# Optimization experiments

Measured on AMD Instinct MI355X. Metric: run time of the kernel, lower is better.

Reference implementation:

```python
import jax, jax.numpy as jnp
import numpy as np

N, E, F, H = 50000, 1_600_000, 6, 64


def setup_inputs() -> dict:
    key = jax.random.key(0)
    ks = jax.random.split(key, 12)
    inp = {
        "vertex_features": jax.random.normal(ks[0], (N, F), dtype=jnp.float32),
        "edges": jax.random.randint(ks[1], (2, E), 0, N, dtype=jnp.int64 if jax.config.jax_enable_x64 else jnp.int32),
        "weights": jax.random.uniform(ks[2], (E,), dtype=jnp.float32),
        # GCNConv layer params (glorot-ish scale) + biases (PyG default bias=True)
        "W1": jax.random.normal(ks[3], (F, H), dtype=jnp.float32) / np.sqrt(F),
        "b1": jnp.zeros((H,), jnp.float32),
        "W2": jax.random.normal(ks[4], (H, H), dtype=jnp.float32) / np.sqrt(H),
        "b2": jnp.zeros((H,), jnp.float32),
        "W3": jax.random.normal(ks[5], (H, H), dtype=jnp.float32) / np.sqrt(H),
        "b3": jnp.zeros((H,), jnp.float32),
        "Wl": jax.random.normal(ks[6], (H, 1), dtype=jnp.float32) / np.sqrt(H),
        "bl": jnp.zeros((1,), jnp.float32),
    }
    return inp


def _gcn_norm(edges, weights, n):
    # PyG gcn_norm: add self loops (weight 1), symmetric D^-1/2 A D^-1/2;
    # degree computed at target nodes (edge_index[1], flow source_to_target).
    row, col = edges[0], edges[1]
    loop = jnp.arange(n, dtype=row.dtype)
    row_f = jnp.concatenate([row, loop])
    col_f = jnp.concatenate([col, loop])
    w_f = jnp.concatenate([weights, jnp.ones((n,), weights.dtype)])
    deg = jax.ops.segment_sum(w_f, col_f, num_segments=n)
    dis = jnp.where(deg > 0, jax.lax.rsqrt(jnp.maximum(deg, 1e-30)), 0.0)
    norm = dis[row_f] * w_f * dis[col_f]
    return row_f, col_f, norm


def _gcn_conv(x, W, b, row, col, norm, n):
    xw = x @ W                                   # [n, H_out]
    agg = jax.ops.segment_sum(norm[:, None] * xw[row], col, num_segments=n)
    return agg + b


def reference(vertex_features, edges, weights, W1, b1, W2, b2, W3, b3, Wl, bl):
    n = vertex_features.shape[0]
    row, col, norm = _gcn_norm(edges, weights, n)  # norm identical for all layers
    h = jax.nn.sigmoid(_gcn_conv(vertex_features, W1, b1, row, col, norm, n))
    h = jax.nn.sigmoid(_gcn_conv(h, W2, b2, row, col, norm, n))
    h = jax.nn.sigmoid(_gcn_conv(h, W3, b3, row, col, norm, n))
    logits = h @ Wl + bl                           # [n, 1]
    return jax.nn.softmax(logits, axis=0)          # softmax over node dim
```

## Files before the change

### kernel.cpp

```cpp
#include <hip/hip_runtime.h>
#include <math.h>


#define BLK 256
#define SKB 256
#define CHUNK 4096

typedef __attribute__((ext_vector_type(8))) short bf16x8;
typedef __attribute__((ext_vector_type(4))) float f32x4;

__device__ inline unsigned short f2bf(float f) {
  unsigned u = __float_as_uint(f);
  return (unsigned short)((u + 0x7FFF + ((u >> 16) & 1)) >> 16);
}
__device__ inline float bflo(unsigned u) { return __uint_as_float(u << 16); }
__device__ inline float bfhi(unsigned u) { return __uint_as_float(u & 0xFFFF0000u); }


__global__ __launch_bounds__(256) void k_binscatter(
    const int* __restrict__ row, const int* __restrict__ col,
    const float* __restrict__ w, int E,
    int* __restrict__ bfill, int2* __restrict__ bucket, int CAP) {
  __shared__ int2 stage[CHUNK];
  __shared__ int lhist[SKB], lbase[SKB], gbase[SKB], lfill[SKB];
  int t = threadIdx.x;
  int e0 = blockIdx.x * CHUNK;
  int n = E - e0; if (n > CHUNK) n = CHUNK;
  lhist[t] = 0; lfill[t] = 0;
  __syncthreads();
  for (int i = t; i < n; i += BLK) atomicAdd(&lhist[((unsigned)col[e0 + i]) >> 8], 1);
  __syncthreads();
  lbase[t] = lhist[t];
  __syncthreads();
  for (int off = 1; off < SKB; off <<= 1) {
    int v = (t >= off) ? lbase[t - off] : 0;
    __syncthreads();
    lbase[t] += v;
    __syncthreads();
  }
  int excl = lbase[t] - lhist[t];
  int cb = lhist[t];
  gbase[t] = cb ? atomicAdd(&bfill[t << 4], cb) : 0;
  __syncthreads();
  lbase[t] = excl;
  __syncthreads();
  for (int i = t; i < n; i += BLK) {
    int c = col[e0 + i];
    int b = ((unsigned)c) >> 8;
    int r = atomicAdd(&lfill[b], 1);
    stage[lbase[b] + r] = make_int2(row[e0 + i] | (c << 16), __float_as_int(w[e0 + i]));
  }
  __syncthreads();
  for (int i = t; i < n; i += BLK) {
    int2 p = stage[i];
    int b = ((unsigned)p.x) >> 24;
    bucket[(size_t)b * CAP + gbase[b] + (i - lbase[b])] = p;
  }
}


__global__ __launch_bounds__(256) void k_build(
    const int2* __restrict__ bucket, const int* __restrict__ bfill,
    const float* __restrict__ x,
    unsigned* __restrict__ csr, int* __restrict__ cnt, int* __restrict__ start,
    float* __restrict__ dis, unsigned short* __restrict__ x8b, int CAP, int N) {
  __shared__ int   hist[SKB];
  __shared__ float wsum[SKB];
  __shared__ int   lstart[SKB + 1];
  __shared__ int   lfill[SKB];
  int b = blockIdx.x, t = threadIdx.x;
  int n0 = b << 8;
  int M = N - n0; if (M > 256) M = 256;
  if (M <= 0) return;
  hist[t] = 0; wsum[t] = 0.0f; lfill[t] = 0;
  __syncthreads();
  const int2* bb = bucket + (size_t)b * CAP;
  int ec = bfill[b << 4];
  for (int i = t; i < ec; i += BLK) {
    int2 p = bb[i];
    int lc = (((unsigned)p.x) >> 16) & 255;
    atomicAdd(&hist[lc], 1);
    atomicAdd(&wsum[lc], __int_as_float(p.y));
  }
  __syncthreads();
  if (t == 0) {
    int run = 0;
    for (int i = 0; i < M; ++i) { lstart[i] = run; run += hist[i]; }
    lstart[M] = run;
  }
  __syncthreads();
  if (t < M) {
    int n = n0 + t;
    cnt[n] = hist[t];
    start[n] = b * CAP + lstart[t];
    float d = 1.0f / sqrtf(wsum[t] + 1.0f);
    dis[n] = d;
    const float* xr = x + (size_t)n * 6;
    uint4 pk;
    pk.x = (unsigned)f2bf(d * xr[0]) | ((unsigned)f2bf(d * xr[1]) << 16);
    pk.y = (unsigned)f2bf(d * xr[2]) | ((unsigned)f2bf(d * xr[3]) << 16);
    pk.z = (unsigned)f2bf(d * xr[4]) | ((unsigned)f2bf(d * xr[5]) << 16);
    pk.w = 0u;
    *(uint4*)(x8b + (size_t)n * 8) = pk;
  }
  __syncthreads();
  for (int i = t; i < ec; i += BLK) {
    int2 p = bb[i];
    int lc = (((unsigned)p.x) >> 16) & 255;
    int pos = lstart[lc] + atomicAdd(&lfill[lc], 1);
    csr[(size_t)b * CAP + pos] =
        ((unsigned)p.x & 0xFFFFu) | ((unsigned)f2bf(__int_as_float(p.y)) << 16);
  }
}


__global__ void k_wprep(const float* __restrict__ W2, const float* __restrict__ W3,
                        unsigned short* __restrict__ W2b, unsigned short* __restrict__ W3b) {
  int i = blockIdx.x * blockDim.x + threadIdx.x;
  if (i < 4096) { W2b[i] = f2bf(W2[i]); W3b[i] = f2bf(W3[i]); }
}


__global__ void k_layer1(const unsigned short* __restrict__ x8b,
                         const int* __restrict__ start, const int* __restrict__ cnt,
                         const unsigned* __restrict__ csr, const float* __restrict__ dis,
                         const float* __restrict__ W1, const float* __restrict__ b1,
                         unsigned short* __restrict__ hb, int N) {
  int t = blockIdx.x * blockDim.x + threadIdx.x;
  int n = t >> 3, sub = t & 7;
  if (n >= N) return;
  float a0 = 0.f, a1 = 0.f, a2 = 0.f, a3 = 0.f, a4 = 0.f, a5 = 0.f;
  if (sub == 0) {
    uint4 sv = *(const uint4*)(x8b + (size_t)n * 8);
    a0 = bflo(sv.x); a1 = bfhi(sv.x); a2 = bflo(sv.y);
    a3 = bfhi(sv.y); a4 = bflo(sv.z); a5 = bfhi(sv.z);
  }
  int s = start[n], e = s + cnt[n];
  int i = s + sub;
  for (; i + 8 < e; i += 16) {
    unsigned p0 = csr[i], p1 = csr[i + 8];
    uint4 h0 = *(const uint4*)(x8b + (size_t)(p0 & 0xFFFFu) * 8);
    uint4 h1 = *(const uint4*)(x8b + (size_t)(p1 & 0xFFFFu) * 8);
    float v0 = bfhi(p0), v1 = bfhi(p1);
    a0 += v0 * bflo(h0.x) + v1 * bflo(h1.x);
    a1 += v0 * bfhi(h0.x) + v1 * bfhi(h1.x);
    a2 += v0 * bflo(h0.y) + v1 * bflo(h1.y);
    a3 += v0 * bfhi(h0.y) + v1 * bfhi(h1.y);
    a4 += v0 * bflo(h0.z) + v1 * bflo(h1.z);
    a5 += v0 * bfhi(h0.z) + v1 * bfhi(h1.z);
  }
  for (; i < e; i += 8) {
    unsigned pe = csr[i];
    float v = bfhi(pe);
    uint4 hv = *(const uint4*)(x8b + (size_t)(pe & 0xFFFFu) * 8);
    a0 += v * bflo(hv.x); a1 += v * bfhi(hv.x);
    a2 += v * bflo(hv.y); a3 += v * bfhi(hv.y);
    a4 += v * bflo(hv.z); a5 += v * bfhi(hv.z);
  }
#pragma unroll
  for (int m = 1; m < 8; m <<= 1) {
    a0 += __shfl_xor(a0, m, 64); a1 += __shfl_xor(a1, m, 64);
    a2 += __shfl_xor(a2, m, 64); a3 += __shfl_xor(a3, m, 64);
    a4 += __shfl_xor(a4, m, 64); a5 += __shfl_xor(a5, m, 64);
  }
  float d = dis[n];
  a0 *= d; a1 *= d; a2 *= d; a3 *= d; a4 *= d; a5 *= d;
  unsigned short* o = hb + (size_t)n * 64;
#pragma unroll
  for (int jj = 0; jj < 2; ++jj) {
    int j4 = sub * 2 + jj;
    float4 acc = *(const float4*)(b1 + j4 * 4);
    const float* Wc = W1 + j4 * 4;
    acc.x += a0*Wc[0] + a1*Wc[64] + a2*Wc[128] + a3*Wc[192] + a4*Wc[256] + a5*Wc[320];
    acc.y += a0*Wc[1] + a1*Wc[65] + a2*Wc[129] + a3*Wc[193] + a4*Wc[257] + a5*Wc[321];
    acc.z += a0*Wc[2] + a1*Wc[66] + a2*Wc[130] + a3*Wc[194] + a4*Wc[258] + a5*Wc[322];
    acc.w += a0*Wc[3] + a1*Wc[67] + a2*Wc[131] + a3*Wc[195] + a4*Wc[259] + a5*Wc[323];
    uint2 pk;
    pk.x = (unsigned)f2bf(d / (1.0f + expf(-acc.x))) |
           ((unsigned)f2bf(d / (1.0f + expf(-acc.y))) << 16);
    pk.y = (unsigned)f2bf(d / (1.0f + expf(-acc.z))) |
           ((unsigned)f2bf(d / (1.0f + expf(-acc.w))) << 16);
    *(uint2*)(o + j4 * 4) = pk;
  }
}


__global__ void k_agg64(const unsigned short* __restrict__ hb,
                        const int* __restrict__ start, const int* __restrict__ cnt,
                        const unsigned* __restrict__ csr, const float* __restrict__ dis,
                        unsigned short* __restrict__ aggb, int N) {
  int t = blockIdx.x * blockDim.x + threadIdx.x;
  int n = t >> 4, sub = t & 15;
  if (n >= N) return;
  uint2 sv = *(const uint2*)(hb + (size_t)n * 64 + sub * 4);
  float a0 = bflo(sv.x), a1 = bfhi(sv.x), a2 = bflo(sv.y), a3 = bfhi(sv.y);
  int s = start[n], e = s + cnt[n];
  int i = s;
  for (; i + 8 <= e; i += 8) {
    unsigned p0 = csr[i],     p1 = csr[i + 1], p2 = csr[i + 2], p3 = csr[i + 3];
    unsigned p4 = csr[i + 4], p5 = csr[i + 5], p6 = csr[i + 6], p7 = csr[i + 7];
    uint2 h0 = *(const uint2*)(hb + (size_t)(p0 & 0xFFFFu) * 64 + sub * 4);
    uint2 h1 = *(const uint2*)(hb + (size_t)(p1 & 0xFFFFu) * 64 + sub * 4);
    uint2 h2 = *(const uint2*)(hb + (size_t)(p2 & 0xFFFFu) * 64 + sub * 4);
    uint2 h3 = *(const uint2*)(hb + (size_t)(p3 & 0xFFFFu) * 64 + sub * 4);
    uint2 h4 = *(const uint2*)(hb + (size_t)(p4 & 0xFFFFu) * 64 + sub * 4);
    uint2 h5 = *(const uint2*)(hb + (size_t)(p5 & 0xFFFFu) * 64 + sub * 4);
    uint2 h6 = *(const uint2*)(hb + (size_t)(p6 & 0xFFFFu) * 64 + sub * 4);
    uint2 h7 = *(const uint2*)(hb + (size_t)(p7 & 0xFFFFu) * 64 + sub * 4);
    float v0 = bfhi(p0), v1 = bfhi(p1), v2 = bfhi(p2), v3 = bfhi(p3);
    float v4 = bfhi(p4), v5 = bfhi(p5), v6 = bfhi(p6), v7 = bfhi(p7);
    a0 += v0*bflo(h0.x) + v1*bflo(h1.x) + v2*bflo(h2.x) + v3*bflo(h3.x)
        + v4*bflo(h4.x) + v5*bflo(h5.x) + v6*bflo(h6.x) + v7*bflo(h7.x);
    a1 += v0*bfhi(h0.x) + v1*bfhi(h1.x) + v2*bfhi(h2.x) + v3*bfhi(h3.x)
        + v4*bfhi(h4.x) + v5*bfhi(h5.x) + v6*bfhi(h6.x) + v7*bfhi(h7.x);
    a2 += v0*bflo(h0.y) + v1*bflo(h1.y) + v2*bflo(h2.y) + v3*bflo(h3.y)
        + v4*bflo(h4.y) + v5*bflo(h5.y) + v6*bflo(h6.y) + v7*bflo(h7.y);
    a3 += v0*bfhi(h0.y) + v1*bfhi(h1.y) + v2*bfhi(h2.y) + v3*bfhi(h3.y)
        + v4*bfhi(h4.y) + v5*bfhi(h5.y) + v6*bfhi(h6.y) + v7*bfhi(h7.y);
  }
  for (; i < e; ++i) {
    unsigned pe = csr[i];
    float v = bfhi(pe);
    uint2 hv = *(const uint2*)(hb + (size_t)(pe & 0xFFFFu) * 64 + sub * 4);
    a0 += v * bflo(hv.x); a1 += v * bfhi(hv.x);
    a2 += v * bflo(hv.y); a3 += v * bfhi(hv.y);
  }
  float d = dis[n];
  uint2 pk;
  pk.x = (unsigned)f2bf(d * a0) | ((unsigned)f2bf(d * a1) << 16);
  pk.y = (unsigned)f2bf(d * a2) | ((unsigned)f2bf(d * a3) << 16);
  *(uint2*)(aggb + (size_t)n * 64 + sub * 4) = pk;
}


__global__ __launch_bounds__(256) void k_dense64_mfma(
    const unsigned short* __restrict__ aggb, const unsigned short* __restrict__ Wb,
    const float* __restrict__ b, const float* __restrict__ dis,
    unsigned short* __restrict__ hb, int NS) {
  int wid = threadIdx.x >> 6, lane = threadIdx.x & 63;
  int quad = lane >> 4, r16 = lane & 15;
  bf16x8 Bf[2][4];
#pragma unroll
  for (int kt = 0; kt < 2; ++kt)
#pragma unroll
    for (int jt = 0; jt < 4; ++jt)
#pragma unroll
      for (int j = 0; j < 8; ++j)
        Bf[kt][jt][j] = (short)Wb[(kt * 32 + quad * 8 + j) * 64 + jt * 16 + r16];
  float bias[4];
#pragma unroll
  for (int jt = 0; jt < 4; ++jt) bias[jt] = b[jt * 16 + r16];
  int stride = gridDim.x * 4;
  for (int s = blockIdx.x * 4 + wid; s < NS; s += stride) {
    int n0 = s * 16;
    bf16x8 Af0 = *(const bf16x8*)(aggb + (size_t)(n0 + r16) * 64 + quad * 8);
    bf16x8 Af1 = *(const bf16x8*)(aggb + (size_t)(n0 + r16) * 64 + 32 + quad * 8);
    f32x4 C[4];
#pragma unroll
    for (int jt = 0; jt < 4; ++jt) {
      f32x4 z = {0.f, 0.f, 0.f, 0.f};
      z = __builtin_amdgcn_mfma_f32_16x16x32_bf16(Af0, Bf[0][jt], z, 0, 0, 0);
      z = __builtin_amdgcn_mfma_f32_16x16x32_bf16(Af1, Bf[1][jt], z, 0, 0, 0);
      C[jt] = z;
    }
    float dv[4];
#pragma unroll
    for (int reg = 0; reg < 4; ++reg) dv[reg] = dis[n0 + quad * 4 + reg];
#pragma unroll
    for (int jt = 0; jt < 4; ++jt)
#pragma unroll
      for (int reg = 0; reg < 4; ++reg) {
        float h = dv[reg] / (1.0f + expf(-(C[jt][reg] + bias[jt])));
        hb[(size_t)(n0 + quad * 4 + reg) * 64 + jt * 16 + r16] = f2bf(h);
      }
  }
}


__global__ __launch_bounds__(256) void k_head_mfma(
    const unsigned short* __restrict__ aggb, const unsigned short* __restrict__ Wb,
    const float* __restrict__ b, const float* __restrict__ Wl,
    const float* __restrict__ bl, float* __restrict__ expv,
    float* __restrict__ red_part, int NS) {
  int wid = threadIdx.x >> 6, lane = threadIdx.x & 63;
  int quad = lane >> 4, r16 = lane & 15;
  bf16x8 Bf[2][4];
#pragma unroll
  for (int kt = 0; kt < 2; ++kt)
#pragma unroll
    for (int jt = 0; jt < 4; ++jt)
#pragma unroll
      for (int j = 0; j < 8; ++j)
        Bf[kt][jt][j] = (short)Wb[(kt * 32 + quad * 8 + j) * 64 + jt * 16 + r16];
  float bias[4], wlv[4];
#pragma unroll
  for (int jt = 0; jt < 4; ++jt) {
    bias[jt] = b[jt * 16 + r16];
    wlv[jt]  = Wl[jt * 16 + r16];
  }
  float bl0 = bl[0];
  float lsum = 0.0f;
  int stride = gridDim.x * 4;
  for (int s = blockIdx.x * 4 + wid; s < NS; s += stride) {
    int n0 = s * 16;
    bf16x8 Af0 = *(const bf16x8*)(aggb + (size_t)(n0 + r16) * 64 + quad * 8);
    bf16x8 Af1 = *(const bf16x8*)(aggb + (size_t)(n0 + r16) * 64 + 32 + quad * 8);
    f32x4 C[4];
#pragma unroll
    for (int jt = 0; jt < 4; ++jt) {
      f32x4 z = {0.f, 0.f, 0.f, 0.f};
      z = __builtin_amdgcn_mfma_f32_16x16x32_bf16(Af0, Bf[0][jt], z, 0, 0, 0);
      z = __builtin_amdgcn_mfma_f32_16x16x32_bf16(Af1, Bf[1][jt], z, 0, 0, 0);
      C[jt] = z;
    }
    float p0 = 0, p1 = 0, p2 = 0, p3 = 0;
#pragma unroll
    for (int jt = 0; jt < 4; ++jt) {
      p0 += wlv[jt] / (1.0f + expf(-(C[jt][0] + bias[jt])));
      p1 += wlv[jt] / (1.0f + expf(-(C[jt][1] + bias[jt])));
      p2 += wlv[jt] / (1.0f + expf(-(C[jt][2] + bias[jt])));
      p3 += wlv[jt] / (1.0f + expf(-(C[jt][3] + bias[jt])));
    }
#pragma unroll
    for (int m = 1; m < 16; m <<= 1) {
      p0 += __shfl_xor(p0, m, 64);
      p1 += __shfl_xor(p1, m, 64);
      p2 += __shfl_xor(p2, m, 64);
      p3 += __shfl_xor(p3, m, 64);
    }
    float ls = 0.0f;
    if (r16 == 0) {
      float e0 = expf(p0 + bl0), e1 = expf(p1 + bl0);
      float e2 = expf(p2 + bl0), e3 = expf(p3 + bl0);
      int r = n0 + quad * 4;
      expv[r] = e0; expv[r + 1] = e1; expv[r + 2] = e2; expv[r + 3] = e3;
      ls = e0 + e1 + e2 + e3;
    }
    ls += __shfl_xor(ls, 16, 64);
    ls += __shfl_xor(ls, 32, 64);
    lsum += ls;
  }
  if (lane == 0) atomicAdd(&red_part[(blockIdx.x & 63) << 4], lsum);
}

__global__ void k_out(const float* __restrict__ expv, int N,
                      const float* __restrict__ red_part, float* __restrict__ out) {
  int i = blockIdx.x * blockDim.x + threadIdx.x;
  int lane = threadIdx.x & 63;
  float s = red_part[lane << 4];
#pragma unroll
  for (int o = 32; o > 0; o >>= 1) s += __shfl_down(s, o, 64);
  s = __shfl(s, 0, 64);
  if (i < N) out[i] = expv[i] / s;
}


extern "C" void kernel_launch(void* const* d_in, const int* in_sizes, int n_in,
                              void* d_out, int out_size, void* d_ws, size_t ws_size,
                              hipStream_t stream) {
  const float* x   = (const float*)d_in[0];
  const int*   edg = (const int*)d_in[1];
  const float* w   = (const float*)d_in[2];
  const float* W1  = (const float*)d_in[3];
  const float* b1  = (const float*)d_in[4];
  const float* W2  = (const float*)d_in[5];
  const float* b2  = (const float*)d_in[6];
  const float* W3  = (const float*)d_in[7];
  const float* b3  = (const float*)d_in[8];
  const float* Wl  = (const float*)d_in[9];
  const float* bl  = (const float*)d_in[10];
  float* out = (float*)d_out;

  const int N = in_sizes[0] / 6;
  const int E = in_sizes[2];
  const int* row = edg;
  const int* col = edg + E;
  const int NB = (N + 255) >> 8;
  const int NS = (N + 15) / 16;

  size_t off = 0;
  char* base = (char*)d_ws;
  auto alloc = [&](size_t bytes) -> void* {
    void* p = base + off;
    off += (bytes + 255) & ~(size_t)255;
    return p;
  };
  int*   bfill    = (int*)alloc((size_t)SKB * 16 * 4);
  float* red_part = (float*)alloc((size_t)64 * 16 * 4);
  size_t zero_bytes = off;
  int*   cnt    = (int*)alloc((size_t)N * 4);
  int*   start  = (int*)alloc((size_t)N * 4);
  float* dis    = (float*)alloc((size_t)N * 4);
  float* expv   = (float*)alloc((size_t)N * 4);
  unsigned short* x8b = (unsigned short*)alloc((size_t)N * 8 * 2);
  unsigned short* hb  = (unsigned short*)alloc((size_t)N * 64 * 2);
  unsigned short* W2b = (unsigned short*)alloc(4096 * 2);
  unsigned short* W3b = (unsigned short*)alloc(4096 * 2);
  size_t remain = (ws_size > off) ? (ws_size - off) : 0;
  long long capn = ((long long)remain) / ((long long)NB * 12);
  int CAP = (int)capn;
  if (CAP > 9216) CAP = 9216;
  if (CAP < 8704) CAP = 8704;
  unsigned* csr = (unsigned*)alloc((size_t)NB * CAP * 4);
  size_t aggsz = (size_t)N * 64 * 2;
  size_t bksz  = (size_t)NB * CAP * 8;
  void* shared_blk = alloc(aggsz > bksz ? aggsz : bksz);
  int2*           bucket = (int2*)shared_blk;
  unsigned short* aggb   = (unsigned short*)shared_blk;

  const int gE   = (E + CHUNK - 1) / CHUNK;
  const int gN   = (N + BLK - 1) / BLK;
  const int gN8  = (N * 8 + BLK - 1) / BLK;
  const int gN16 = (N * 16 + BLK - 1) / BLK;
  const int gM   = 200;

  hipMemsetAsync(d_ws, 0, zero_bytes, stream);

  k_wprep     <<<16, BLK, 0, stream>>>(W2, W3, W2b, W3b);
  k_binscatter<<<gE, BLK, 0, stream>>>(row, col, w, E, bfill, bucket, CAP);
  k_build     <<<NB, BLK, 0, stream>>>(bucket, bfill, x, csr, cnt, start, dis, x8b, CAP, N);

  k_layer1<<<gN8, BLK, 0, stream>>>(x8b, start, cnt, csr, dis, W1, b1, hb, N);

  k_agg64       <<<gN16, BLK, 0, stream>>>(hb, start, cnt, csr, dis, aggb, N);
  k_dense64_mfma<<<gM,   BLK, 0, stream>>>(aggb, W2b, b2, dis, hb, NS);

  k_agg64    <<<gN16, BLK, 0, stream>>>(hb, start, cnt, csr, dis, aggb, N);
  k_head_mfma<<<gM,   BLK, 0, stream>>>(aggb, W3b, b3, Wl, bl, expv, red_part, NS);

  k_out<<<gN, BLK, 0, stream>>>(expv, N, red_part, out);
}
```

Before: 234.7 us.

## Fuse neighbor aggregation with MFMA dense transform per 16-node tile

Merges the separate aggregation and MFMA dense kernels for layers 2 and 3 into single kernels. Each block aggregates 16 nodes into padded shared memory, then runs the 64x64 bf16 MFMA and sigmoid, and for the last layer also the head, exp and partial sum. This removes the global round trip of the aggregated buffer and two launches. Layer 2 now writes to a separate buffer that reuses the bucket space, because other blocks still read the input features. The weight-conversion kernel is folded into extra blocks of the bin-scatter launch. The trade-off is that each block now reloads W from global memory and the head does more atomics, one per 16 nodes.

```diff
diff --git a/kernel.cpp b/kernel.cpp
--- a/kernel.cpp
+++ b/kernel.cpp
@@ -5,6 +5,7 @@
 #define BLK 256
 #define SKB 256
 #define CHUNK 4096
+#define LROW 72
 
 typedef __attribute__((ext_vector_type(8))) short bf16x8;
 typedef __attribute__((ext_vector_type(4))) float f32x4;
@@ -20,7 +21,14 @@
 __global__ __launch_bounds__(256) void k_binscatter(
     const int* __restrict__ row, const int* __restrict__ col,
     const float* __restrict__ w, int E,
-    int* __restrict__ bfill, int2* __restrict__ bucket, int CAP) {
+    int* __restrict__ bfill, int2* __restrict__ bucket, int CAP, int nEB,
+    const float* __restrict__ W2, const float* __restrict__ W3,
+    unsigned short* __restrict__ W2b, unsigned short* __restrict__ W3b) {
+  if (blockIdx.x >= nEB) {
+    int i = (blockIdx.x - nEB) * BLK + threadIdx.x;
+    if (i < 4096) { W2b[i] = f2bf(W2[i]); W3b[i] = f2bf(W3[i]); }
+    return;
+  }
   __shared__ int2 stage[CHUNK];
   __shared__ int lhist[SKB], lbase[SKB], gbase[SKB], lfill[SKB];
   int t = threadIdx.x;
@@ -114,13 +122,6 @@
 }
 
 
-__global__ void k_wprep(const float* __restrict__ W2, const float* __restrict__ W3,
-                        unsigned short* __restrict__ W2b, unsigned short* __restrict__ W3b) {
-  int i = blockIdx.x * blockDim.x + threadIdx.x;
-  if (i < 4096) { W2b[i] = f2bf(W2[i]); W3b[i] = f2bf(W3[i]); }
-}
-
-
 __global__ void k_layer1(const unsigned short* __restrict__ x8b,
                          const int* __restrict__ start, const int* __restrict__ cnt,
                          const unsigned* __restrict__ csr, const float* __restrict__ dis,
@@ -185,162 +186,143 @@
 }
 
 
-__global__ void k_agg64(const unsigned short* __restrict__ hb,
-                        const int* __restrict__ start, const int* __restrict__ cnt,
-                        const unsigned* __restrict__ csr, const float* __restrict__ dis,
-                        unsigned short* __restrict__ aggb, int N) {
-  int t = blockIdx.x * blockDim.x + threadIdx.x;
-  int n = t >> 4, sub = t & 15;
-  if (n >= N) return;
-  uint2 sv = *(const uint2*)(hb + (size_t)n * 64 + sub * 4);
-  float a0 = bflo(sv.x), a1 = bfhi(sv.x), a2 = bflo(sv.y), a3 = bfhi(sv.y);
-  int s = start[n], e = s + cnt[n];
-  int i = s;
-  for (; i + 8 <= e; i += 8) {
-    unsigned p0 = csr[i],     p1 = csr[i + 1], p2 = csr[i + 2], p3 = csr[i + 3];
-    unsigned p4 = csr[i + 4], p5 = csr[i + 5], p6 = csr[i + 6], p7 = csr[i + 7];
-    uint2 h0 = *(const uint2*)(hb + (size_t)(p0 & 0xFFFFu) * 64 + sub * 4);
-    uint2 h1 = *(const uint2*)(hb + (size_t)(p1 & 0xFFFFu) * 64 + sub * 4);
-    uint2 h2 = *(const uint2*)(hb + (size_t)(p2 & 0xFFFFu) * 64 + sub * 4);
-    uint2 h3 = *(const uint2*)(hb + (size_t)(p3 & 0xFFFFu) * 64 + sub * 4);
-    uint2 h4 = *(const uint2*)(hb + (size_t)(p4 & 0xFFFFu) * 64 + sub * 4);
-    uint2 h5 = *(const uint2*)(hb + (size_t)(p5 & 0xFFFFu) * 64 + sub * 4);
-    uint2 h6 = *(const uint2*)(hb + (size_t)(p6 & 0xFFFFu) * 64 + sub * 4);
-    uint2 h7 = *(const uint2*)(hb + (size_t)(p7 & 0xFFFFu) * 64 + sub * 4);
-    float v0 = bfhi(p0), v1 = bfhi(p1), v2 = bfhi(p2), v3 = bfhi(p3);
-    float v4 = bfhi(p4), v5 = bfhi(p5), v6 = bfhi(p6), v7 = bfhi(p7);
-    a0 += v0*bflo(h0.x) + v1*bflo(h1.x) + v2*bflo(h2.x) + v3*bflo(h3.x)
-        + v4*bflo(h4.x) + v5*bflo(h5.x) + v6*bflo(h6.x) + v7*bflo(h7.x);
-    a1 += v0*bfhi(h0.x) + v1*bfhi(h1.x) + v2*bfhi(h2.x) + v3*bfhi(h3.x)
-        + v4*bfhi(h4.x) + v5*bfhi(h5.x) + v6*bfhi(h6.x) + v7*bfhi(h7.x);
-    a2 += v0*bflo(h0.y) + v1*bflo(h1.y) + v2*bflo(h2.y) + v3*bflo(h3.y)
-        + v4*bflo(h4.y) + v5*bflo(h5.y) + v6*bflo(h6.y) + v7*bflo(h7.y);
-    a3 += v0*bfhi(h0.y) + v1*bfhi(h1.y) + v2*bfhi(h2.y) + v3*bfhi(h3.y)
-        + v4*bfhi(h4.y) + v5*bfhi(h5.y) + v6*bfhi(h6.y) + v7*bfhi(h7.y);
-  }
-  for (; i < e; ++i) {
-    unsigned pe = csr[i];
-    float v = bfhi(pe);
-    uint2 hv = *(const uint2*)(hb + (size_t)(pe & 0xFFFFu) * 64 + sub * 4);
-    a0 += v * bflo(hv.x); a1 += v * bfhi(hv.x);
-    a2 += v * bflo(hv.y); a3 += v * bfhi(hv.y);
-  }
-  float d = dis[n];
-  uint2 pk;
-  pk.x = (unsigned)f2bf(d * a0) | ((unsigned)f2bf(d * a1) << 16);
-  pk.y = (unsigned)f2bf(d * a2) | ((unsigned)f2bf(d * a3) << 16);
-  *(uint2*)(aggb + (size_t)n * 64 + sub * 4) = pk;
-}
-
-
-__global__ __launch_bounds__(256) void k_dense64_mfma(
-    const unsigned short* __restrict__ aggb, const unsigned short* __restrict__ Wb,
-    const float* __restrict__ b, const float* __restrict__ dis,
-    unsigned short* __restrict__ hb, int NS) {
-  int wid = threadIdx.x >> 6, lane = threadIdx.x & 63;
-  int quad = lane >> 4, r16 = lane & 15;
-  bf16x8 Bf[2][4];
-#pragma unroll
-  for (int kt = 0; kt < 2; ++kt)
-#pragma unroll
-    for (int jt = 0; jt < 4; ++jt)
-#pragma unroll
-      for (int j = 0; j < 8; ++j)
-        Bf[kt][jt][j] = (short)Wb[(kt * 32 + quad * 8 + j) * 64 + jt * 16 + r16];
-  float bias[4];
-#pragma unroll
-  for (int jt = 0; jt < 4; ++jt) bias[jt] = b[jt * 16 + r16];
-  int stride = gridDim.x * 4;
-  for (int s = blockIdx.x * 4 + wid; s < NS; s += stride) {
-    int n0 = s * 16;
-    bf16x8 Af0 = *(const bf16x8*)(aggb + (size_t)(n0 + r16) * 64 + quad * 8);
-    bf16x8 Af1 = *(const bf16x8*)(aggb + (size_t)(n0 + r16) * 64 + 32 + quad * 8);
-    f32x4 C[4];
-#pragma unroll
-    for (int jt = 0; jt < 4; ++jt) {
-      f32x4 z = {0.f, 0.f, 0.f, 0.f};
-      z = __builtin_amdgcn_mfma_f32_16x16x32_bf16(Af0, Bf[0][jt], z, 0, 0, 0);
-      z = __builtin_amdgcn_mfma_f32_16x16x32_bf16(Af1, Bf[1][jt], z, 0, 0, 0);
-      C[jt] = z;
+__device__ inline void agg16(const unsigned short* __restrict__ hb,
+                             const int* __restrict__ start,
+                             const int* __restrict__ cnt,
+                             const unsigned* __restrict__ csr,
+                             const float* __restrict__ dis,
+                             unsigned short* lag, int n0, int N) {
+  int t = threadIdx.x;
+  int r = t >> 4, sub = t & 15;
+  int n = n0 + r;
+  uint2 pk = make_uint2(0u, 0u);
+  if (n < N) {
+    uint2 sv = *(const uint2*)(hb + (size_t)n * 64 + sub * 4);
+    float a0 = bflo(sv.x), a1 = bfhi(sv.x), a2 = bflo(sv.y), a3 = bfhi(sv.y);
+    int s = start[n], e = s + cnt[n];
+    int i = s;
+    for (; i + 8 <= e; i += 8) {
+      unsigned p0 = csr[i],     p1 = csr[i + 1], p2 = csr[i + 2], p3 = csr[i + 3];
+      unsigned p4 = csr[i + 4], p5 = csr[i + 5], p6 = csr[i + 6], p7 = csr[i + 7];
+      uint2 h0 = *(const uint2*)(hb + (size_t)(p0 & 0xFFFFu) * 64 + sub * 4);
+      uint2 h1 = *(const uint2*)(hb + (size_t)(p1 & 0xFFFFu) * 64 + sub * 4);
+      uint2 h2 = *(const uint2*)(hb + (size_t)(p2 & 0xFFFFu) * 64 + sub * 4);
+      uint2 h3 = *(const uint2*)(hb + (size_t)(p3 & 0xFFFFu) * 64 + sub * 4);
+      uint2 h4 = *(const uint2*)(hb + (size_t)(p4 & 0xFFFFu) * 64 + sub * 4);
+      uint2 h5 = *(const uint2*)(hb + (size_t)(p5 & 0xFFFFu) * 64 + sub * 4);
+      uint2 h6 = *(const uint2*)(hb + (size_t)(p6 & 0xFFFFu) * 64 + sub * 4);
+      uint2 h7 = *(const uint2*)(hb + (size_t)(p7 & 0xFFFFu) * 64 + sub * 4);
+      float v0 = bfhi(p0), v1 = bfhi(p1), v2 = bfhi(p2), v3 = bfhi(p3);
+      float v4 = bfhi(p4), v5 = bfhi(p5), v6 = bfhi(p6), v7 = bfhi(p7);
+      a0 += v0*bflo(h0.x) + v1*bflo(h1.x) + v2*bflo(h2.x) + v3*bflo(h3.x)
+          + v4*bflo(h4.x) + v5*bflo(h5.x) + v6*bflo(h6.x) + v7*bflo(h7.x);
+      a1 += v0*bfhi(h0.x) + v1*bfhi(h1.x) + v2*bfhi(h2.x) + v3*bfhi(h3.x)
+          + v4*bfhi(h4.x) + v5*bfhi(h5.x) + v6*bfhi(h6.x) + v7*bfhi(h7.x);
+      a2 += v0*bflo(h0.y) + v1*bflo(h1.y) + v2*bflo(h2.y) + v3*bflo(h3.y)
+          + v4*bflo(h4.y) + v5*bflo(h5.y) + v6*bflo(h6.y) + v7*bflo(h7.y);
+      a3 += v0*bfhi(h0.y) + v1*bfhi(h1.y) + v2*bfhi(h2.y) + v3*bfhi(h3.y)
+          + v4*bfhi(h4.y) + v5*bfhi(h5.y) + v6*bfhi(h6.y) + v7*bfhi(h7.y);
     }
-    float dv[4];
-#pragma unroll
-    for (int reg = 0; reg < 4; ++reg) dv[reg] = dis[n0 + quad * 4 + reg];
-#pragma unroll
-    for (int jt = 0; jt < 4; ++jt)
-#pragma unroll
-      for (int reg = 0; reg < 4; ++reg) {
-        float h = dv[reg] / (1.0f + expf(-(C[jt][reg] + bias[jt])));
-        hb[(size_t)(n0 + quad * 4 + reg) * 64 + jt * 16 + r16] = f2bf(h);
-      }
-  }
-}
-
-
-__global__ __launch_bounds__(256) void k_head_mfma(
-    const unsigned short* __restrict__ aggb, const unsigned short* __restrict__ Wb,
-    const float* __restrict__ b, const float* __restrict__ Wl,
-    const float* __restrict__ bl, float* __restrict__ expv,
-    float* __restrict__ red_part, int NS) {
-  int wid = threadIdx.x >> 6, lane = threadIdx.x & 63;
-  int quad = lane >> 4, r16 = lane & 15;
-  bf16x8 Bf[2][4];
-#pragma unroll
-  for (int kt = 0; kt < 2; ++kt)
-#pragma unroll
-    for (int jt = 0; jt < 4; ++jt)
-#pragma unroll
-      for (int j = 0; j < 8; ++j)
-        Bf[kt][jt][j] = (short)Wb[(kt * 32 + quad * 8 + j) * 64 + jt * 16 + r16];
-  float bias[4], wlv[4];
-#pragma unroll
-  for (int jt = 0; jt < 4; ++jt) {
-    bias[jt] = b[jt * 16 + r16];
-    wlv[jt]  = Wl[jt * 16 + r16];
-  }
-  float bl0 = bl[0];
-  float lsum = 0.0f;
-  int stride = gridDim.x * 4;
-  for (int s = blockIdx.x * 4 + wid; s < NS; s += stride) {
-    int n0 = s * 16;
-    bf16x8 Af0 = *(const bf16x8*)(aggb + (size_t)(n0 + r16) * 64 + quad * 8);
-    bf16x8 Af1 = *(const bf16x8*)(aggb + (size_t)(n0 + r16) * 64 + 32 + quad * 8);
-    f32x4 C[4];
-#pragma unroll
-    for (int jt = 0; jt < 4; ++jt) {
-      f32x4 z = {0.f, 0.f, 0.f, 0.f};
-      z = __builtin_amdgcn_mfma_f32_16x16x32_bf16(Af0, Bf[0][jt], z, 0, 0, 0);
-      z = __builtin_amdgcn_mfma_f32_16x16x32_bf16(Af1, Bf[1][jt], z, 0, 0, 0);
-      C[jt] = z;
+    for (; i < e; ++i) {
+      unsigned pe = csr[i];
+      float v = bfhi(pe);
+      uint2 hv = *(const uint2*)(hb + (size_t)(pe & 0xFFFFu) * 64 + sub * 4);
+      a0 += v * bflo(hv.x); a1 += v * bfhi(hv.x);
+      a2 += v * bflo(hv.y); a3 += v * bfhi(hv.y);
     }
-    float p0 = 0, p1 = 0, p2 = 0, p3 = 0;
-#pragma unroll
-    for (int jt = 0; jt < 4; ++jt) {
-      p0 += wlv[jt] / (1.0f + expf(-(C[jt][0] + bias[jt])));
-      p1 += wlv[jt] / (1.0f + expf(-(C[jt][1] + bias[jt])));
-      p2 += wlv[jt] / (1.0f + expf(-(C[jt][2] + bias[jt])));
-      p3 += wlv[jt] / (1.0f + expf(-(C[jt][3] + bias[jt])));
+    float d = dis[n];
+    pk.x = (unsigned)f2bf(d * a0) | ((unsigned)f2bf(d * a1) << 16);
+    pk.y = (unsigned)f2bf(d * a2) | ((unsigned)f2bf(d * a3) << 16);
+  }
+  *(uint2*)(lag + r * LROW + sub * 4) = pk;
+}
+
+
+__global__ __launch_bounds__(256) void k_layer2f(
+    const unsigned short* __restrict__ hb_in,
+    const int* __restrict__ start, const int* __restrict__ cnt,
+    const unsigned* __restrict__ csr, const float* __restrict__ dis,
+    const unsigned short* __restrict__ Wb, const float* __restrict__ b,
+    unsigned short* __restrict__ hb_out, int N) {
+  __shared__ unsigned short lag[16 * LROW];
+  int n0 = blockIdx.x * 16;
+  agg16(hb_in, start, cnt, csr, dis, lag, n0, N);
+  __syncthreads();
+  int t = threadIdx.x;
+  int wid = t >> 6, lane = t & 63, quad = lane >> 4, r16 = lane & 15;
+  bf16x8 Af0 = *(const bf16x8*)(lag + r16 * LROW + quad * 8);
+  bf16x8 Af1 = *(const bf16x8*)(lag + r16 * LROW + 32 + quad * 8);
+  bf16x8 Bf0, Bf1;
+#pragma unroll
+  for (int j = 0; j < 8; ++j) {
+    Bf0[j] = (short)Wb[(quad * 8 + j) * 64 + wid * 16 + r16];
+    Bf1[j] = (short)Wb[(32 + quad * 8 + j) * 64 + wid * 16 + r16];
+  }
+  f32x4 z = {0.f, 0.f, 0.f, 0.f};
+  z = __builtin_amdgcn_mfma_f32_16x16x32_bf16(Af0, Bf0, z, 0, 0, 0);
+  z = __builtin_amdgcn_mfma_f32_16x16x32_bf16(Af1, Bf1, z, 0, 0, 0);
+  float bias = b[wid * 16 + r16];
+#pragma unroll
+  for (int reg = 0; reg < 4; ++reg) {
+    int nb = n0 + quad * 4 + reg;
+    if (nb < N) {
+      float h = dis[nb] / (1.0f + expf(-(z[reg] + bias)));
+      hb_out[(size_t)nb * 64 + wid * 16 + r16] = f2bf(h);
     }
-#pragma unroll
-    for (int m = 1; m < 16; m <<= 1) {
-      p0 += __shfl_xor(p0, m, 64);
-      p1 += __shfl_xor(p1, m, 64);
-      p2 += __shfl_xor(p2, m, 64);
-      p3 += __shfl_xor(p3, m, 64);
-    }
-    float ls = 0.0f;
-    if (r16 == 0) {
-      float e0 = expf(p0 + bl0), e1 = expf(p1 + bl0);
-      float e2 = expf(p2 + bl0), e3 = expf(p3 + bl0);
-      int r = n0 + quad * 4;
-      expv[r] = e0; expv[r + 1] = e1; expv[r + 2] = e2; expv[r + 3] = e3;
-      ls = e0 + e1 + e2 + e3;
-    }
-    ls += __shfl_xor(ls, 16, 64);
-    ls += __shfl_xor(ls, 32, 64);
-    lsum += ls;
-  }
-  if (lane == 0) atomicAdd(&red_part[(blockIdx.x & 63) << 4], lsum);
+  }
+}
+
+
+__global__ __launch_bounds__(256) void k_layer3f(
+    const unsigned short* __restrict__ hb_in,
+    const int* __restrict__ start, const int* __restrict__ cnt,
+    const unsigned* __restrict__ csr, const float* __restrict__ dis,
+    const unsigned short* __restrict__ Wb, const float* __restrict__ b,
+    const float* __restrict__ Wl, const float* __restrict__ bl,
+    float* __restrict__ expv, float* __restrict__ red_part, int N) {
+  __shared__ unsigned short lag[16 * LROW];
+  __shared__ float psum[16][4];
+  int n0 = blockIdx.x * 16;
+  agg16(hb_in, start, cnt, csr, dis, lag, n0, N);
+  __syncthreads();
+  int t = threadIdx.x;
+  int wid = t >> 6, lane = t & 63, quad = lane >> 4, r16 = lane & 15;
+  bf16x8 Af0 = *(const bf16x8*)(lag + r16 * LROW + quad * 8);
+  bf16x8 Af1 = *(const bf16x8*)(lag + r16 * LROW + 32 + quad * 8);
+  bf16x8 Bf0, Bf1;
+#pragma unroll
+  for (int j = 0; j < 8; ++j) {
+    Bf0[j] = (short)Wb[(quad * 8 + j) * 64 + wid * 16 + r16];
+    Bf1[j] = (short)Wb[(32 + quad * 8 + j) * 64 + wid * 16 + r16];
+  }
+  f32x4 z = {0.f, 0.f, 0.f, 0.f};
+  z = __builtin_amdgcn_mfma_f32_16x16x32_bf16(Af0, Bf0, z, 0, 0, 0);
+  z = __builtin_amdgcn_mfma_f32_16x16x32_bf16(Af1, Bf1, z, 0, 0, 0);
+  float bias = b[wid * 16 + r16];
+  float wl = Wl[wid * 16 + r16];
+  float p[4];
+#pragma unroll
+  for (int reg = 0; reg < 4; ++reg)
+    p[reg] = wl / (1.0f + expf(-(z[reg] + bias)));
+#pragma unroll
+  for (int m = 1; m < 16; m <<= 1) {
+#pragma unroll
+    for (int reg = 0; reg < 4; ++reg) p[reg] += __shfl_xor(p[reg], m, 64);
+  }
+  if (r16 == 0) {
+#pragma unroll
+    for (int reg = 0; reg < 4; ++reg) psum[quad * 4 + reg][wid] = p[reg];
+  }
+  __syncthreads();
+  if (t < 16) {
+    int n = n0 + t;
+    float lg = psum[t][0] + psum[t][1] + psum[t][2] + psum[t][3] + bl[0];
+    float ev = (n < N) ? expf(lg) : 0.f;
+    if (n < N) expv[n] = ev;
+#pragma unroll
+    for (int m = 1; m < 16; m <<= 1) ev += __shfl_xor(ev, m, 64);
+    if (t == 0) atomicAdd(&red_part[(blockIdx.x & 63) << 4], ev);
+  }
 }
 
 __global__ void k_out(const float* __restrict__ expv, int N,
@@ -376,7 +358,6 @@
   const int* row = edg;
   const int* col = edg + E;
   const int NB = (N + 255) >> 8;
-  const int NS = (N + 15) / 16;
 
   size_t off = 0;
   char* base = (char*)d_ws;
@@ -402,31 +383,30 @@
   if (CAP > 9216) CAP = 9216;
   if (CAP < 8704) CAP = 8704;
   unsigned* csr = (unsigned*)alloc((size_t)NB * CAP * 4);
-  size_t aggsz = (size_t)N * 64 * 2;
-  size_t bksz  = (size_t)NB * CAP * 8;
-  void* shared_blk = alloc(aggsz > bksz ? aggsz : bksz);
+  size_t h2sz = (size_t)N * 64 * 2;
+  size_t bksz = (size_t)NB * CAP * 8;
+  void* shared_blk = alloc(h2sz > bksz ? h2sz : bksz);
   int2*           bucket = (int2*)shared_blk;
-  unsigned short* aggb   = (unsigned short*)shared_blk;
-
-  const int gE   = (E + CHUNK - 1) / CHUNK;
-  const int gN   = (N + BLK - 1) / BLK;
-  const int gN8  = (N * 8 + BLK - 1) / BLK;
-  const int gN16 = (N * 16 + BLK - 1) / BLK;
-  const int gM   = 200;
+  unsigned short* hb2    = (unsigned short*)shared_blk;
+
+  const int nEB = (E + CHUNK - 1) / CHUNK;
+  const int gE  = nEB + 16;
+  const int gN  = (N + BLK - 1) / BLK;
+  const int gN8 = (N * 8 + BLK - 1) / BLK;
+  const int g16 = (N + 15) / 16;
 
   hipMemsetAsync(d_ws, 0, zero_bytes, stream);
 
-  k_wprep     <<<16, BLK, 0, stream>>>(W2, W3, W2b, W3b);
-  k_binscatter<<<gE, BLK, 0, stream>>>(row, col, w, E, bfill, bucket, CAP);
+  k_binscatter<<<gE, BLK, 0, stream>>>(row, col, w, E, bfill, bucket, CAP,
+                                       nEB, W2, W3, W2b, W3b);
   k_build     <<<NB, BLK, 0, stream>>>(bucket, bfill, x, csr, cnt, start, dis, x8b, CAP, N);
 
   k_layer1<<<gN8, BLK, 0, stream>>>(x8b, start, cnt, csr, dis, W1, b1, hb, N);
 
-  k_agg64       <<<gN16, BLK, 0, stream>>>(hb, start, cnt, csr, dis, aggb, N);
-  k_dense64_mfma<<<gM,   BLK, 0, stream>>>(aggb, W2b, b2, dis, hb, NS);
-
-  k_agg64    <<<gN16, BLK, 0, stream>>>(hb, start, cnt, csr, dis, aggb, N);
-  k_head_mfma<<<gM,   BLK, 0, stream>>>(aggb, W3b, b3, Wl, bl, expv, red_part, NS);
+  k_layer2f<<<g16, BLK, 0, stream>>>(hb, start, cnt, csr, dis, W2b, b2, hb2, N);
+
+  k_layer3f<<<g16, BLK, 0, stream>>>(hb2, start, cnt, csr, dis, W3b, b3,
+                                     Wl, bl, expv, red_part, N);
 
   k_out<<<gN, BLK, 0, stream>>>(expv, N, red_part, out);
 }
```

Result: faster. 216.3 us, median of 2 (-7.9%).
